# Optimization experiments

Hardware: AMD Instinct MI355X
Metric: run time of the kernel (lower is better)

Reference implementation:

```python
import jax, jax.numpy as jnp
import numpy as np

DIM_IN = 128; DIM_OUT = 128; DIM_X = 256; L = 256
BATCH = 8192; STD = 0.5; EPS = 1e-3; CRL = 1.0


def setup_inputs() -> dict:
    key = jax.random.key(0)
    ks = jax.random.split(key, 9)
    n = 2 * DIM_X + L
    # trainable params (as in torch __init__)
    X   = jax.random.normal(ks[0], (n, n)) * STD
    Y   = jax.random.normal(ks[1], (DIM_X, DIM_X)) * STD
    B2  = jax.random.normal(ks[2], (DIM_X, DIM_IN)) * STD
    C2  = jax.random.normal(ks[3], (DIM_OUT, DIM_X)) * STD
    D21 = jax.random.normal(ks[4], (DIM_OUT, L)) * STD
    D22 = jax.random.normal(ks[5], (DIM_OUT, DIM_IN)) * STD
    D12 = jax.random.normal(ks[6], (L, DIM_IN)) * STD
    # derived params per update_model_param (stored detached in the torch module)
    H = X.T @ X + EPS * jnp.eye(n)
    H11 = H[:DIM_X, :DIM_X]
    H21 = H[DIM_X:DIM_X + L, :DIM_X]
    H22 = H[DIM_X:DIM_X + L, DIM_X:DIM_X + L]
    H31 = H[DIM_X + L:, :DIM_X]
    H32 = H[DIM_X + L:, DIM_X:DIM_X + L]
    H33 = H[DIM_X + L:, DIM_X + L:]
    Fm  = H31
    B1  = H32
    E   = 0.5 * (H11 + CRL * H33 + Y - Y.T)
    Lam = 0.5 * jnp.diag(H22)            # positive diagonal of Lambda
    D11 = -jnp.tril(H22, -1)             # strictly lower triangular
    C1  = -H21
    x    = jax.random.normal(ks[7], (1, 1, DIM_X)) * 0.1   # internal state (broadcast over batch)
    u_in = jax.random.normal(ks[8], (BATCH, 1, DIM_IN))
    return {"u_in": u_in, "x": x, "Fm": Fm, "B1": B1, "B2": B2, "C1": C1,
            "C2": C2, "D11": D11, "D12": D12, "D21": D21, "D22": D22,
            "E": E, "Lam": Lam}


def ren_forward(u_in, x, Fm, B1, B2, C1, C2, D11, D12, D21, D22, E, Lam):
    batch = u_in.shape[0]
    l = Lam.shape[0]
    # per-step affine terms that do not depend on w (hoisted out of the loop)
    cx = jnp.einsum('li,aoi->l', C1, x)         # (l,)   x has leading dims (1,1)
    du = jnp.einsum('li,boi->lbo', D12, u_in)   # (l,B,1)
    eye = jnp.eye(l, dtype=u_in.dtype)
    w0 = jnp.zeros((batch, 1, l), u_in.dtype)

    # sequential forward substitution: D11 is strictly lower triangular, so
    # step i only reads w columns < i and writes column i.
    def step(w, inp):
        d11_i, lam_i, cx_i, du_i, e_i = inp
        v = cx_i + jnp.einsum('bol,l->bo', w, d11_i) + du_i   # (B,1)
        w = w + e_i * jnp.tanh(v / lam_i)[..., None]          # write column i
        return w, None

    w, _ = jax.lax.scan(step, w0, (D11, Lam, cx, du, eye))    # (B,1,l)

    Einv_T = jnp.linalg.inv(E).T
    x_new = (jnp.einsum('aoi,ji->aoj', x, Fm)
             + jnp.einsum('bol,jl->boj', w, B1)
             + jnp.einsum('boi,ji->boj', u_in, B2)) @ Einv_T  # (B,1,dim_x)
    y = x_new @ C2.T + w @ D21.T + u_in @ D22.T               # (B,1,dim_out)
    return y


def reference(u_in, x, Fm, B1, B2, C1, C2, D11, D12, D21, D22, E, Lam):
    return ren_forward(u_in, x, Fm, B1, B2, C1, C2, D11, D12, D21, D22, E, Lam)
```

## Files before the change

### kernel.cpp

```cpp
#include <hip/hip_runtime.h>
#include <utility>

#define NB 8192

template <typename F, size_t... I>
__device__ __forceinline__ void sfor_impl(F&& f, std::index_sequence<I...>) {
  (f(std::integral_constant<int, (int)I>{}), ...);
}
template <int N, typename F>
__device__ __forceinline__ void sfor(F&& f) {
  sfor_impl((F&&)f, std::make_index_sequence<N>{});
}

constexpr int coff(int li) {
  int o = 0;
  for (int j = 0; j < li; ++j) o += ((63 - j) + 3) & ~3;
  return o;
}
#define CPACK_STRIDE 2176

__device__ __forceinline__ float fast_rcp(float x) {
  float r = __builtin_amdgcn_rcpf(x);
  return r * (2.0f - x * r);
}

__device__ __forceinline__ float fast_tanh(float x) {
  const float e = __expf(2.0f * fminf(x, 40.0f));
  return 1.0f - 2.0f * fast_rcp(e + 1.0f);
}


__device__ void dev_prep(const float* __restrict__ x, const float* __restrict__ C1,
                         const float* __restrict__ Fm, const float* __restrict__ Lam,
                         float* __restrict__ cx, float* __restrict__ xF,
                         float* __restrict__ rLam, int t) {
  float s1 = 0.f, s2 = 0.f;
  for (int i = 0; i < 256; ++i) {
    const float xi = x[i];
    s1 += C1[t * 256 + i] * xi;
    s2 += Fm[t * 256 + i] * xi;
  }
  cx[t] = s1;
  xF[t] = s2;
  rLam[t] = 1.0f / Lam[t];
}

__device__ void dev_pack(const float* __restrict__ D11, float* __restrict__ cpack,
                         int t) {
  const int c = t >> 6;
  const int lane = t & 63;
  int off = 0;
  for (int li = 0; li < 63; ++li) {
    if (lane < 63 - li)
      cpack[c * CPACK_STRIDE + off + lane] =
          D11[(c * 64 + li + 1 + lane) * 256 + (c * 64 + li)];
    off += ((63 - li) + 3) & ~3;
  }
}

__device__ void dev_inv(const float* __restrict__ srcT, int ld,
                        float* __restrict__ dstT, int tid) {
  __shared__ float Pcols[128][20];
  __shared__ float MB[128][20];
  __shared__ float Ar[16][132];
  __shared__ float invD[16 * 20];
  const int ti = tid >> 5;
  const int tj = tid & 31;
  const int R = ti * 8, C = tj * 4;
  float a[8][4];
#pragma unroll
  for (int j = 0; j < 4; ++j)
#pragma unroll
    for (int g = 0; g < 2; ++g) {
      const float4 v = *(const float4*)&srcT[(C + j) * ld + (R + 4 * g)];
      a[4 * g + 0][j] = v.x; a[4 * g + 1][j] = v.y;
      a[4 * g + 2][j] = v.z; a[4 * g + 3][j] = v.w;
    }

  for (int s = 0; s < 8; ++s) {
    if ((tj >> 2) == s) {
      const int c0 = C - 16 * s;
#pragma unroll
      for (int i = 0; i < 8; ++i)
        *(float4*)&Pcols[R + i][c0] =
            make_float4(a[i][0], a[i][1], a[i][2], a[i][3]);
    }
    if ((ti >> 1) == s) {
      const int r0 = R - 16 * s;
#pragma unroll
      for (int i = 0; i < 8; ++i)
        *(float4*)&Ar[r0 + i][C] =
            make_float4(a[i][0], a[i][1], a[i][2], a[i][3]);
    }
    __syncthreads();

    if (tid < 16) {
      float q[16];
#pragma unroll
      for (int g = 0; g < 4; ++g) {
        const float4 v = *(const float4*)&Pcols[s * 16 + tid][4 * g];
        q[4 * g] = v.x; q[4 * g + 1] = v.y; q[4 * g + 2] = v.z; q[4 * g + 3] = v.w;
      }
#pragma unroll
      for (int kk = 0; kk < 16; ++kk) {
        float ps[16];
#pragma unroll
        for (int j = 0; j < 16; ++j)
          ps[j] = __int_as_float(
              __builtin_amdgcn_readlane(__float_as_int(q[j]), kk));
        const float piv = fast_rcp(ps[kk]);
#pragma unroll
        for (int j = 0; j < 16; ++j) ps[j] = (j == kk) ? piv : ps[j] * piv;
        const bool isP = (tid == kk);
        const float te = isP ? -1.0f : q[kk];
#pragma unroll
        for (int j = 0; j < 16; ++j) {
          const float base = (isP || j == kk) ? 0.0f : q[j];
          q[j] = base - te * ps[j];
        }
      }
#pragma unroll
      for (int g = 0; g < 4; ++g)
        *(float4*)&invD[tid * 20 + 4 * g] =
            make_float4(q[4 * g], q[4 * g + 1], q[4 * g + 2], q[4 * g + 3]);
    }
    __syncthreads();

    {
      const int r = tid & 127, h = tid >> 7;
      float4 mv;
      if ((r >> 4) == s) {
        mv = *(const float4*)&invD[(r & 15) * 20 + 4 * h];
      } else {
        mv = make_float4(0.f, 0.f, 0.f, 0.f);
#pragma unroll
        for (int g = 0; g < 4; ++g) {
          const float4 p = *(const float4*)&Pcols[r][4 * g];
          const float pc[4] = {p.x, p.y, p.z, p.w};
#pragma unroll
          for (int q = 0; q < 4; ++q) {
            const float4 d = *(const float4*)&invD[(4 * g + q) * 20 + 4 * h];
            mv.x -= pc[q] * d.x; mv.y -= pc[q] * d.y;
            mv.z -= pc[q] * d.z; mv.w -= pc[q] * d.w;
          }
        }
      }
      *(float4*)&MB[r][4 * h] = mv;
    }
    __syncthreads();

    if ((tj >> 2) == s) {
      const int c0 = C - 16 * s;
#pragma unroll
      for (int i = 0; i < 8; ++i) {
        const float4 m = *(const float4*)&MB[R + i][c0];
        a[i][0] = m.x; a[i][1] = m.y; a[i][2] = m.z; a[i][3] = m.w;
      }
    } else {
      if ((ti >> 1) == s) {
#pragma unroll
        for (int i = 0; i < 8; ++i)
#pragma unroll
          for (int j = 0; j < 4; ++j) a[i][j] = 0.f;
      }
#pragma unroll
      for (int half = 0; half < 2; ++half) {
        float4 ar[8];
#pragma unroll
        for (int k = 0; k < 8; ++k)
          ar[k] = *(const float4*)&Ar[half * 8 + k][C];
#pragma unroll
        for (int i = 0; i < 8; ++i) {
          const float4 m0 = *(const float4*)&MB[R + i][half * 8];
          const float4 m1 = *(const float4*)&MB[R + i][half * 8 + 4];
          const float mi[8] = {m0.x, m0.y, m0.z, m0.w, m1.x, m1.y, m1.z, m1.w};
#pragma unroll
          for (int k = 0; k < 8; ++k) {
            a[i][0] += mi[k] * ar[k].x;
            a[i][1] += mi[k] * ar[k].y;
            a[i][2] += mi[k] * ar[k].z;
            a[i][3] += mi[k] * ar[k].w;
          }
        }
      }
    }
    __syncthreads();
  }
#pragma unroll
  for (int j = 0; j < 4; ++j)
#pragma unroll
    for (int g = 0; g < 2; ++g)
      *(float4*)&dstT[(C + j) * 128 + (R + 4 * g)] = make_float4(
          a[4 * g + 0][j], a[4 * g + 1][j], a[4 * g + 2][j], a[4 * g + 3][j]);
}

__device__ void dev_T(const float* __restrict__ u, float* __restrict__ vw, int bid,
                      int t) {
  __shared__ float buf[64 * 65];
  const int b0 = bid * 64;
#pragma unroll
  for (int h = 0; h < 2; ++h) {
#pragma unroll
    for (int q = 0; q < 8; ++q) {
      const int idx = q * 512 + t;
      const int bl = idx >> 6;
      const int i2 = idx & 63;
      buf[i2 * 65 + bl] = u[(b0 + bl) * 128 + 64 * h + i2];
    }
    __syncthreads();
#pragma unroll
    for (int q = 0; q < 8; ++q) {
      const int idx = q * 512 + t;
      const int i2 = idx >> 6;
      const int bl = idx & 63;
      vw[(256 + 64 * h + i2) * NB + b0 + bl] = buf[i2 * 65 + bl];
    }
    __syncthreads();
  }
}

__device__ void dev_du(const float* __restrict__ D12, const float* __restrict__ cx,
                       float* __restrict__ vw, int bid, int t) {
  __shared__ float Dl[8 * 128];
  const int bx = bid & 7;
  const int l0 = (bid >> 3) * 8;
#pragma unroll
  for (int q = 0; q < 4; ++q) Dl[q * 256 + t] = D12[l0 * 128 + q * 256 + t];
  __syncthreads();
  const float4* vw4 = (const float4*)vw;
  float4* vw4o = (float4*)vw;
  const int b4 = bx * 256 + t;
  float4 acc[8];
#pragma unroll
  for (int j = 0; j < 8; ++j) {
    const float cj = cx[l0 + j];
    acc[j] = make_float4(cj, cj, cj, cj);
  }
#pragma unroll 4
  for (int i = 0; i < 128; ++i) {
    const float4 wv = vw4[(256 + i) * 2048 + b4];
#pragma unroll
    for (int j = 0; j < 8; ++j) {
      const float d = Dl[j * 128 + i];
      acc[j].x += d * wv.x;
      acc[j].y += d * wv.y;
      acc[j].z += d * wv.z;
      acc[j].w += d * wv.w;
    }
  }
#pragma unroll
  for (int j = 0; j < 8; ++j) vw4o[(l0 + j) * 2048 + b4] = acc[j];
}

__device__ void dev_WZ(const float* __restrict__ E, const float* __restrict__ C2,
                       const float* __restrict__ inv1T, float* __restrict__ W,
                       float* __restrict__ z1, int gid) {
  const int half = gid >> 14;
  const int idx = gid & 16383;
  const int j = idx >> 7;
  const int i = idx & 127;
  float s = 0.f;
  if (half == 0) {
    for (int m = 0; m < 128; ++m) s += inv1T[m * 128 + i] * E[(128 + j) * 256 + m];
    W[i * 128 + j] = s;
  } else {
    for (int m = 0; m < 128; ++m) s += inv1T[m * 128 + i] * C2[j * 256 + m];
    z1[i * 128 + j] = s;
  }
}

__device__ void dev_SC(const float* __restrict__ E, const float* __restrict__ C2,
                       const float* __restrict__ W, const float* __restrict__ z1,
                       float* __restrict__ STt, float* __restrict__ c2p, int gid) {
  if (gid < 16384) {
    const int jj = gid >> 7;
    const int i = gid & 127;
    float s = E[(128 + jj) * 256 + 128 + i];
    for (int m = 0; m < 128; ++m) s -= E[m * 256 + 128 + i] * W[m * 128 + jj];
    STt[jj * 128 + i] = s;
  } else {
    const int idx = gid - 16384;
    const int i = idx >> 7;
    const int o = idx & 127;
    float s = C2[o * 256 + 128 + i];
    for (int m = 0; m < 128; ++m) s -= E[m * 256 + 128 + i] * z1[m * 128 + o];
    c2p[i * 128 + o] = s;
  }
}

__device__ void dev_G2(const float* __restrict__ inv2T, const float* __restrict__ c2p,
                       float* __restrict__ g2, int gid) {
  const int i = gid >> 7;
  const int o = gid & 127;
  float s = 0.f;
  for (int m = 0; m < 128; ++m) s += inv2T[m * 128 + i] * c2p[m * 128 + o];
  g2[i * 128 + o] = s;
}

__device__ void dev_G1(const float* __restrict__ W, const float* __restrict__ z1,
                       const float* __restrict__ g2, float* __restrict__ g1, int gid) {
  const int i = gid >> 7;
  const int o = gid & 127;
  float s = z1[i * 128 + o];
  for (int m = 0; m < 128; ++m) s -= W[i * 128 + m] * g2[m * 128 + o];
  g1[i * 128 + o] = s;
}

__device__ void dev_R(const float* __restrict__ B1, const float* __restrict__ B2,
                      const float* __restrict__ D21, const float* __restrict__ D22,
                      const float* __restrict__ g1, const float* __restrict__ g2,
                      const float* __restrict__ xF, float* __restrict__ R,
                      float* __restrict__ y0, int gid) {
  if (gid < 32768) {
    const int o = gid >> 8;
    const int l = gid & 255;
    float s = D21[o * 256 + l];
    for (int m = 0; m < 128; ++m) {
      s += g1[m * 128 + o] * B1[m * 256 + l];
      s += g2[m * 128 + o] * B1[(128 + m) * 256 + l];
    }
    R[o * 384 + l] = s;
  } else if (gid < 49152) {
    const int t2 = gid - 32768;
    const int o = t2 >> 7;
    const int i = t2 & 127;
    float s = D22[o * 128 + i];
    for (int m = 0; m < 128; ++m) {
      s += g1[m * 128 + o] * B2[m * 128 + i];
      s += g2[m * 128 + o] * B2[(128 + m) * 128 + i];
    }
    R[o * 384 + 256 + i] = s;
  } else if (gid < 49280) {
    const int o = gid - 49152;
    float s = 0.f;
    for (int m = 0; m < 128; ++m) {
      s += g1[m * 128 + o] * xF[m];
      s += g2[m * 128 + o] * xF[128 + m];
    }
    y0[o] = s;
  }
}

__device__ void dev_scan(const float* __restrict__ cpack,
                         const float* __restrict__ rLam, float* __restrict__ vw,
                         int c, int bid, int t) {
  const int b = bid * 256 + t;
  const int l0 = c * 64;
  const float4* cp4 = (const float4*)(cpack + c * CPACK_STRIDE);
  float v[64];
#pragma unroll
  for (int li = 0; li < 64; ++li) v[li] = vw[(l0 + li) * NB + b];
  sfor<64>([&](auto LI) {
    constexpr int li = decltype(LI)::value;
    const float w = fast_tanh(v[li] * rLam[l0 + li]);
    vw[(l0 + li) * NB + b] = w;
    constexpr int n = 63 - li;
    constexpr int off4 = coff(li) / 4;
    sfor<(n + 3) / 4>([&](auto Q) {
      constexpr int q = decltype(Q)::value;
      const float4 d = cp4[off4 + q];
      if constexpr (4 * q + 0 < n) v[li + 1 + 4 * q + 0] += d.x * w;
      if constexpr (4 * q + 1 < n) v[li + 1 + 4 * q + 1] += d.y * w;
      if constexpr (4 * q + 2 < n) v[li + 1 + 4 * q + 2] += d.z * w;
      if constexpr (4 * q + 3 < n) v[li + 1 + 4 * q + 3] += d.w * w;
    });
  });
}

__device__ void dev_upd(const float* __restrict__ D11, float* __restrict__ vw, int c,
                        int bid, int t) {
  float4* vw4 = (float4*)vw;
  const int b4 = (bid & 7) * 256 + t;
  const int lp0 = (c + 1) * 64 + (bid >> 3) * 8;
  const int k0 = c * 64;
  float4 acc[8];
#pragma unroll
  for (int j = 0; j < 8; ++j) acc[j] = vw4[(lp0 + j) * 2048 + b4];
  for (int k = 0; k < 64; ++k) {
    const float4 wv = vw4[(k0 + k) * 2048 + b4];
#pragma unroll
    for (int j = 0; j < 8; ++j) {
      const float d = D11[(lp0 + j) * 256 + k0 + k];
      acc[j].x += d * wv.x;
      acc[j].y += d * wv.y;
      acc[j].z += d * wv.z;
      acc[j].w += d * wv.w;
    }
  }
#pragma unroll
  for (int j = 0; j < 8; ++j) vw4[(lp0 + j) * 2048 + b4] = acc[j];
}


__global__ __launch_bounds__(512) void mega1(const float* u, const float* x,
                                             const float* C1, const float* Fm,
                                             const float* Lam, const float* D11,
                                             const float* E, float* vw, float* cx,
                                             float* xF, float* rLam, float* cpack,
                                             float* inv1T) {
  const int bid = blockIdx.x;
  const int t = threadIdx.x;
  if (bid < 128) {
    dev_T(u, vw, bid, t);
  } else if (bid == 128) {
    if (t < 256) dev_prep(x, C1, Fm, Lam, cx, xF, rLam, t);
  } else if (bid == 129) {
    if (t < 256) dev_pack(D11, cpack, t);
  } else {
    dev_inv(E, 256, inv1T, t);
  }
}

__global__ __launch_bounds__(256) void mega2(const float* D12, const float* cx,
                                             float* vw, const float* E,
                                             const float* C2, const float* inv1T,
                                             float* W, float* z1) {
  const int bid = blockIdx.x;
  const int t = threadIdx.x;
  if (bid < 256) dev_du(D12, cx, vw, bid, t);
  else dev_WZ(E, C2, inv1T, W, z1, (bid - 256) * 256 + t);
}

__global__ __launch_bounds__(256) void mega3(const float* cpack, const float* rLam,
                                             float* vw, const float* E,
                                             const float* C2, const float* W,
                                             const float* z1, float* STt,
                                             float* c2p) {
  const int bid = blockIdx.x;
  const int t = threadIdx.x;
  if (bid < 32) dev_scan(cpack, rLam, vw, 0, bid, t);
  else dev_SC(E, C2, W, z1, STt, c2p, (bid - 32) * 256 + t);
}

__global__ __launch_bounds__(512) void mega4(const float* D11, float* vw,
                                             const float* STt, float* inv2T) {
  const int bid = blockIdx.x;
  const int t = threadIdx.x;
  if (bid < 96) {
    dev_upd(D11, vw, 0, bid * 2 + (t >> 8), t & 255);
  } else {
    dev_inv(STt, 128, inv2T, t);
  }
}

__global__ __launch_bounds__(256) void mega5(const float* cpack, const float* rLam,
                                             float* vw, const float* inv2T,
                                             const float* c2p, float* g2) {
  const int bid = blockIdx.x;
  const int t = threadIdx.x;
  if (bid < 32) dev_scan(cpack, rLam, vw, 1, bid, t);
  else dev_G2(inv2T, c2p, g2, (bid - 32) * 256 + t);
}

__global__ __launch_bounds__(256) void mega6(const float* D11, float* vw,
                                             const float* W, const float* z1,
                                             const float* g2, float* g1) {
  const int bid = blockIdx.x;
  const int t = threadIdx.x;
  if (bid < 128) dev_upd(D11, vw, 1, bid, t);
  else dev_G1(W, z1, g2, g1, (bid - 128) * 256 + t);
}

__global__ __launch_bounds__(256) void mega7(const float* cpack, const float* rLam,
                                             float* vw, const float* B1,
                                             const float* B2, const float* D21,
                                             const float* D22, const float* g1,
                                             const float* g2, const float* xF,
                                             float* R, float* y0) {
  const int bid = blockIdx.x;
  const int t = threadIdx.x;
  if (bid < 32) dev_scan(cpack, rLam, vw, 2, bid, t);
  else dev_R(B1, B2, D21, D22, g1, g2, xF, R, y0, (bid - 32) * 256 + t);
}

__global__ __launch_bounds__(256) void mega8(const float* D11, float* vw) {
  dev_upd(D11, vw, 2, blockIdx.x, threadIdx.x);
}

__global__ __launch_bounds__(256) void mega9(const float* cpack, const float* rLam,
                                             float* vw) {
  dev_scan(cpack, rLam, vw, 3, blockIdx.x, threadIdx.x);
}

__global__ __launch_bounds__(256) void k_y(const float* __restrict__ vw,
                                           const float* __restrict__ R,
                                           const float* __restrict__ y0,
                                           float* __restrict__ y) {
  __shared__ float Rl[1536];
  const int tid = threadIdx.x;
  const int bid = blockIdx.x;
  const int gx = bid & 7;
  const int gy = bid >> 3;
  const int o0 = gy * 4;
#pragma unroll
  for (int q = 0; q < 6; ++q) Rl[q * 256 + tid] = R[o0 * 384 + q * 256 + tid];
  __syncthreads();

  const float4* vw4 = (const float4*)vw;
  const int b4 = gx * 256 + tid;
  float acc[4][4];
#pragma unroll
  for (int j = 0; j < 4; ++j) {
    const float y0j = y0[o0 + j];
#pragma unroll
    for (int bi = 0; bi < 4; ++bi) acc[bi][j] = y0j;
  }
#pragma unroll 4
  for (int k = 0; k < 384; k += 4) {
    const float4 w0 = vw4[(k + 0) * 2048 + b4];
    const float4 w1 = vw4[(k + 1) * 2048 + b4];
    const float4 w2 = vw4[(k + 2) * 2048 + b4];
    const float4 w3 = vw4[(k + 3) * 2048 + b4];
#pragma unroll
    for (int j = 0; j < 4; ++j) {
      const float4 r = *(const float4*)&Rl[j * 384 + k];
      acc[0][j] += r.x * w0.x + r.y * w1.x + r.z * w2.x + r.w * w3.x;
      acc[1][j] += r.x * w0.y + r.y * w1.y + r.z * w2.y + r.w * w3.y;
      acc[2][j] += r.x * w0.z + r.y * w1.z + r.z * w2.z + r.w * w3.z;
      acc[3][j] += r.x * w0.w + r.y * w1.w + r.z * w2.w + r.w * w3.w;
    }
  }
  const int b0 = b4 * 4;
#pragma unroll
  for (int bi = 0; bi < 4; ++bi) {
    *(float4*)&y[(b0 + bi) * 128 + o0] =
        make_float4(acc[bi][0], acc[bi][1], acc[bi][2], acc[bi][3]);
  }
}

extern "C" void kernel_launch(void* const* d_in, const int* in_sizes, int n_in,
                              void* d_out, int out_size, void* d_ws, size_t ws_size,
                              hipStream_t stream) {
  const float* u   = (const float*)d_in[0];
  const float* x   = (const float*)d_in[1];
  const float* Fm  = (const float*)d_in[2];
  const float* B1  = (const float*)d_in[3];
  const float* B2  = (const float*)d_in[4];
  const float* C1  = (const float*)d_in[5];
  const float* C2  = (const float*)d_in[6];
  const float* D11 = (const float*)d_in[7];
  const float* D12 = (const float*)d_in[8];
  const float* D21 = (const float*)d_in[9];
  const float* D22 = (const float*)d_in[10];
  const float* E   = (const float*)d_in[11];
  const float* Lam = (const float*)d_in[12];
  float* y = (float*)d_out;

  float* F = (float*)d_ws;
  float* vw    = F;
  float* SMb   = F + 384 * NB;
  float* inv1T = SMb;
  float* Wm    = SMb + 16384;
  float* z1    = SMb + 32768;
  float* STt   = SMb + 49152;
  float* c2p   = SMb + 65536;
  float* inv2T = SMb + 81920;
  float* g2    = SMb + 98304;
  float* g1    = SMb + 114688;
  float* Rm    = SMb + 131072;
  float* y0v   = SMb + 180224;
  float* cx    = SMb + 180352;
  float* xF    = SMb + 180608;
  float* rLam  = SMb + 180864;
  float* cpack = SMb + 181120;

  mega1<<<131, 512, 0, stream>>>(u, x, C1, Fm, Lam, D11, E, vw, cx, xF, rLam,
                                 cpack, inv1T);
  mega2<<<384, 256, 0, stream>>>(D12, cx, vw, E, C2, inv1T, Wm, z1);
  mega3<<<160, 256, 0, stream>>>(cpack, rLam, vw, E, C2, Wm, z1, STt, c2p);
  mega4<<<97, 512, 0, stream>>>(D11, vw, STt, inv2T);
  mega5<<<96, 256, 0, stream>>>(cpack, rLam, vw, inv2T, c2p, g2);
  mega6<<<192, 256, 0, stream>>>(D11, vw, Wm, z1, g2, g1);
  mega7<<<225, 256, 0, stream>>>(cpack, rLam, vw, B1, B2, D21, D22, g1, g2, xF,
                                 Rm, y0v);
  mega8<<<64, 256, 0, stream>>>(D11, vw);
  mega9<<<32, 256, 0, stream>>>(cpack, rLam, vw);
  k_y<<<256, 256, 0, stream>>>(vw, Rm, y0v, y);
}
```

Measured before the change: 365.2 us.

## Split matrix inversions across kernels to rebalance side work against the scan chain

```diff
diff --git a/kernel.cpp b/kernel.cpp
--- a/kernel.cpp
+++ b/kernel.cpp
@@ -59,7 +59,7 @@
 }
 
 __device__ void dev_inv(const float* __restrict__ srcT, int ld,
-                        float* __restrict__ dstT, int tid) {
+                        float* __restrict__ dstT, int tid, int s0, int s1) {
   __shared__ float Pcols[128][20];
   __shared__ float MB[128][20];
   __shared__ float Ar[16][132];
@@ -77,7 +77,7 @@
       a[4 * g + 2][j] = v.z; a[4 * g + 3][j] = v.w;
     }
 
-  for (int s = 0; s < 8; ++s) {
+  for (int s = s0; s < s1; ++s) {
     if ((tj >> 2) == s) {
       const int c0 = C - 16 * s;
 #pragma unroll
@@ -219,17 +219,17 @@
   }
 }
 
-__device__ void dev_du(const float* __restrict__ D12, const float* __restrict__ cx,
-                       float* __restrict__ vw, int bid, int t) {
+__device__ void dev_du512(const float* __restrict__ D12, const float* __restrict__ cx,
+                          float* __restrict__ vw, int bid, int t) {
   __shared__ float Dl[8 * 128];
-  const int bx = bid & 7;
-  const int l0 = (bid >> 3) * 8;
-#pragma unroll
-  for (int q = 0; q < 4; ++q) Dl[q * 256 + t] = D12[l0 * 128 + q * 256 + t];
+  const int bx = bid & 3;
+  const int l0 = (bid >> 2) * 8;
+#pragma unroll
+  for (int q = 0; q < 2; ++q) Dl[q * 512 + t] = D12[l0 * 128 + q * 512 + t];
   __syncthreads();
   const float4* vw4 = (const float4*)vw;
   float4* vw4o = (float4*)vw;
-  const int b4 = bx * 256 + t;
+  const int b4 = bx * 512 + t;
   float4 acc[8];
 #pragma unroll
   for (int j = 0; j < 8; ++j) {
@@ -343,8 +343,8 @@
 
 __device__ void dev_scan(const float* __restrict__ cpack,
                          const float* __restrict__ rLam, float* __restrict__ vw,
-                         int c, int bid, int t) {
-  const int b = bid * 256 + t;
+                         int c, int role, int lane) {
+  const int b = role * 256 + lane;
   const int l0 = c * 64;
   const float4* cp4 = (const float4*)(cpack + c * CPACK_STRIDE);
   float v[64];
@@ -368,10 +368,10 @@
 }
 
 __device__ void dev_upd(const float* __restrict__ D11, float* __restrict__ vw, int c,
-                        int bid, int t) {
+                        int role, int lane) {
   float4* vw4 = (float4*)vw;
-  const int b4 = (bid & 7) * 256 + t;
-  const int lp0 = (c + 1) * 64 + (bid >> 3) * 8;
+  const int b4 = (role & 7) * 256 + lane;
+  const int lp0 = (c + 1) * 64 + (role >> 3) * 8;
   const int k0 = c * 64;
   float4 acc[8];
 #pragma unroll
@@ -397,7 +397,7 @@
                                              const float* Lam, const float* D11,
                                              const float* E, float* vw, float* cx,
                                              float* xF, float* rLam, float* cpack,
-                                             float* inv1T) {
+                                             float* invSt) {
   const int bid = blockIdx.x;
   const int t = threadIdx.x;
   if (bid < 128) {
@@ -407,61 +407,75 @@
   } else if (bid == 129) {
     if (t < 256) dev_pack(D11, cpack, t);
   } else {
-    dev_inv(E, 256, inv1T, t);
-  }
-}
-
-__global__ __launch_bounds__(256) void mega2(const float* D12, const float* cx,
+    dev_inv(E, 256, invSt, t, 0, 4);
+  }
+}
+
+__global__ __launch_bounds__(512) void mega2(const float* D12, const float* cx,
+                                             float* vw, const float* invSt,
+                                             float* inv1T) {
+  const int bid = blockIdx.x;
+  const int t = threadIdx.x;
+  if (bid < 128) dev_du512(D12, cx, vw, bid, t);
+  else dev_inv(invSt, 128, inv1T, t, 4, 8);
+}
+
+__global__ __launch_bounds__(512) void mega3(const float* cpack, const float* rLam,
                                              float* vw, const float* E,
                                              const float* C2, const float* inv1T,
                                              float* W, float* z1) {
   const int bid = blockIdx.x;
   const int t = threadIdx.x;
-  if (bid < 256) dev_du(D12, cx, vw, bid, t);
-  else dev_WZ(E, C2, inv1T, W, z1, (bid - 256) * 256 + t);
-}
-
-__global__ __launch_bounds__(256) void mega3(const float* cpack, const float* rLam,
-                                             float* vw, const float* E,
-                                             const float* C2, const float* W,
-                                             const float* z1, float* STt,
-                                             float* c2p) {
-  const int bid = blockIdx.x;
-  const int t = threadIdx.x;
-  if (bid < 32) dev_scan(cpack, rLam, vw, 0, bid, t);
-  else dev_SC(E, C2, W, z1, STt, c2p, (bid - 32) * 256 + t);
+  if (bid < 16) dev_scan(cpack, rLam, vw, 0, bid * 2 + (t >> 8), t & 255);
+  else dev_WZ(E, C2, inv1T, W, z1, (bid - 16) * 512 + t);
 }
 
 __global__ __launch_bounds__(512) void mega4(const float* D11, float* vw,
-                                             const float* STt, float* inv2T) {
-  const int bid = blockIdx.x;
-  const int t = threadIdx.x;
-  if (bid < 96) {
-    dev_upd(D11, vw, 0, bid * 2 + (t >> 8), t & 255);
-  } else {
-    dev_inv(STt, 128, inv2T, t);
-  }
-}
-
-__global__ __launch_bounds__(256) void mega5(const float* cpack, const float* rLam,
+                                             const float* E, const float* C2,
+                                             const float* W, const float* z1,
+                                             float* STt, float* c2p) {
+  const int bid = blockIdx.x;
+  const int t = threadIdx.x;
+  if (bid < 96) dev_upd(D11, vw, 0, bid * 2 + (t >> 8), t & 255);
+  else dev_SC(E, C2, W, z1, STt, c2p, (bid - 96) * 512 + t);
+}
+
+__global__ __launch_bounds__(512) void mega5(const float* cpack, const float* rLam,
+                                             float* vw, const float* STt,
+                                             float* inv2St) {
+  const int bid = blockIdx.x;
+  const int t = threadIdx.x;
+  if (bid < 16) dev_scan(cpack, rLam, vw, 1, bid * 2 + (t >> 8), t & 255);
+  else dev_inv(STt, 128, inv2St, t, 0, 4);
+}
+
+__global__ __launch_bounds__(512) void mega6(const float* D11, float* vw,
+                                             const float* inv2St, float* inv2T) {
+  const int bid = blockIdx.x;
+  const int t = threadIdx.x;
+  if (bid < 64) dev_upd(D11, vw, 1, bid * 2 + (t >> 8), t & 255);
+  else dev_inv(inv2St, 128, inv2T, t, 4, 8);
+}
+
+__global__ __launch_bounds__(512) void mega7(const float* cpack, const float* rLam,
                                              float* vw, const float* inv2T,
                                              const float* c2p, float* g2) {
   const int bid = blockIdx.x;
   const int t = threadIdx.x;
-  if (bid < 32) dev_scan(cpack, rLam, vw, 1, bid, t);
-  else dev_G2(inv2T, c2p, g2, (bid - 32) * 256 + t);
-}
-
-__global__ __launch_bounds__(256) void mega6(const float* D11, float* vw,
+  if (bid < 16) dev_scan(cpack, rLam, vw, 2, bid * 2 + (t >> 8), t & 255);
+  else dev_G2(inv2T, c2p, g2, (bid - 16) * 512 + t);
+}
+
+__global__ __launch_bounds__(512) void mega8(const float* D11, float* vw,
                                              const float* W, const float* z1,
                                              const float* g2, float* g1) {
   const int bid = blockIdx.x;
   const int t = threadIdx.x;
-  if (bid < 128) dev_upd(D11, vw, 1, bid, t);
-  else dev_G1(W, z1, g2, g1, (bid - 128) * 256 + t);
-}
-
-__global__ __launch_bounds__(256) void mega7(const float* cpack, const float* rLam,
+  if (bid < 32) dev_upd(D11, vw, 2, bid * 2 + (t >> 8), t & 255);
+  else dev_G1(W, z1, g2, g1, (bid - 32) * 512 + t);
+}
+
+__global__ __launch_bounds__(512) void mega9(const float* cpack, const float* rLam,
                                              float* vw, const float* B1,
                                              const float* B2, const float* D21,
                                              const float* D22, const float* g1,
@@ -469,17 +483,8 @@
                                              float* R, float* y0) {
   const int bid = blockIdx.x;
   const int t = threadIdx.x;
-  if (bid < 32) dev_scan(cpack, rLam, vw, 2, bid, t);
-  else dev_R(B1, B2, D21, D22, g1, g2, xF, R, y0, (bid - 32) * 256 + t);
-}
-
-__global__ __launch_bounds__(256) void mega8(const float* D11, float* vw) {
-  dev_upd(D11, vw, 2, blockIdx.x, threadIdx.x);
-}
-
-__global__ __launch_bounds__(256) void mega9(const float* cpack, const float* rLam,
-                                             float* vw) {
-  dev_scan(cpack, rLam, vw, 3, blockIdx.x, threadIdx.x);
+  if (bid < 16) dev_scan(cpack, rLam, vw, 3, bid * 2 + (t >> 8), t & 255);
+  else dev_R(B1, B2, D21, D22, g1, g2, xF, R, y0, (bid - 16) * 512 + t);
 }
 
 __global__ __launch_bounds__(256) void k_y(const float* __restrict__ vw,
@@ -563,17 +568,19 @@
   float* xF    = SMb + 180608;
   float* rLam  = SMb + 180864;
   float* cpack = SMb + 181120;
+  float* invSt  = STt;
+  float* inv2St = g1;
 
   mega1<<<131, 512, 0, stream>>>(u, x, C1, Fm, Lam, D11, E, vw, cx, xF, rLam,
-                                 cpack, inv1T);
-  mega2<<<384, 256, 0, stream>>>(D12, cx, vw, E, C2, inv1T, Wm, z1);
-  mega3<<<160, 256, 0, stream>>>(cpack, rLam, vw, E, C2, Wm, z1, STt, c2p);
-  mega4<<<97, 512, 0, stream>>>(D11, vw, STt, inv2T);
-  mega5<<<96, 256, 0, stream>>>(cpack, rLam, vw, inv2T, c2p, g2);
-  mega6<<<192, 256, 0, stream>>>(D11, vw, Wm, z1, g2, g1);
-  mega7<<<225, 256, 0, stream>>>(cpack, rLam, vw, B1, B2, D21, D22, g1, g2, xF,
+                                 cpack, invSt);
+  mega2<<<129, 512, 0, stream>>>(D12, cx, vw, invSt, inv1T);
+  mega3<<<80, 512, 0, stream>>>(cpack, rLam, vw, E, C2, inv1T, Wm, z1);
+  mega4<<<160, 512, 0, stream>>>(D11, vw, E, C2, Wm, z1, STt, c2p);
+  mega5<<<17, 512, 0, stream>>>(cpack, rLam, vw, STt, inv2St);
+  mega6<<<65, 512, 0, stream>>>(D11, vw, inv2St, inv2T);
+  mega7<<<48, 512, 0, stream>>>(cpack, rLam, vw, inv2T, c2p, g2);
+  mega8<<<64, 512, 0, stream>>>(D11, vw, Wm, z1, g2, g1);
+  mega9<<<113, 512, 0, stream>>>(cpack, rLam, vw, B1, B2, D21, D22, g1, g2, xF,
                                  Rm, y0v);
-  mega8<<<64, 256, 0, stream>>>(D11, vw);
-  mega9<<<32, 256, 0, stream>>>(cpack, rLam, vw);
   k_y<<<256, 256, 0, stream>>>(vw, Rm, y0v, y);
 }
```

Result: slower. 422.9 us (+15.8%).
